# Performance work log

Hardware: AMD Instinct MI355X
Metric: run time of the kernel (lower is better)

The kernel has to match this reference:

```python
import jax, jax.numpy as jnp
import numpy as np

H = 16  # n_heads

def setup_inputs() -> dict:
    key = jax.random.key(0)
    ks = jax.random.split(key, 8)
    B, S, D = 2, 2048, 1024
    q = jax.random.normal(ks[0], (B, S, D), dtype=jnp.float32)
    k = jax.random.normal(ks[1], (B, S, D), dtype=jnp.float32)
    v = jax.random.normal(ks[2], (B, S, D), dtype=jnp.float32)
    mask = jnp.ones((B, S, S), dtype=jnp.int32)
    scale = 1.0 / np.sqrt(D)
    Wq = jax.random.normal(ks[3], (D, D), dtype=jnp.float32) * scale
    Wk = jax.random.normal(ks[4], (D, D), dtype=jnp.float32) * scale
    Wv = jax.random.normal(ks[5], (D, D), dtype=jnp.float32) * scale
    Wo = jax.random.normal(ks[6], (D, D), dtype=jnp.float32) * scale
    return {"q": q, "k": k, "v": v, "mask": mask,
            "Wq": Wq, "Wk": Wk, "Wv": Wv, "Wo": Wo}

def reference(q, k, v, mask, Wq, Wk, Wv, Wo):
    B, S, D = q.shape
    dk = D // H
    # nn.Linear(bias=False): y = x @ W.T
    query = (q @ Wq.T).reshape(B, S, H, dk).transpose(0, 2, 1, 3)  # [B,H,S,dk]
    key_  = (k @ Wk.T).reshape(B, S, H, dk).transpose(0, 2, 1, 3)
    value = (v @ Wv.T).reshape(B, S, H, dk).transpose(0, 2, 1, 3)
    scores = jnp.einsum('bhqd,bhkd->bhqk', query, key_) / jnp.sqrt(jnp.float32(dk))
    scores = jnp.where(mask[:, None, :, :] == 0, jnp.float32(-1e9), scores)
    attn = jax.nn.softmax(scores, axis=-1)  # dropout=0.0 -> identity
    x = jnp.einsum('bhqk,bhkd->bhqd', attn, value)  # [B,H,S,dk]
    x = x.transpose(0, 2, 1, 3).reshape(B, S, D)
    return x @ Wo.T
```

## Files before the change

kernel.cpp:

```cpp
#include <hip/hip_runtime.h>
#include <hip/hip_bf16.h>

#define B_ 2
#define S_ 2048
#define D_ 1024
#define H_ 16

typedef __bf16 bf16x8 __attribute__((ext_vector_type(8)));
typedef __bf16 bf16x4v __attribute__((ext_vector_type(4)));
typedef float f32x4 __attribute__((ext_vector_type(4)));
typedef float f32x16 __attribute__((ext_vector_type(16)));

__device__ __forceinline__ float exp2fast(float x) {
  return __builtin_amdgcn_exp2f(x);
}

__device__ __forceinline__ unsigned short f2bf(float f) {
  unsigned int u = __float_as_uint(f);
  u += 0x7fff + ((u >> 16) & 1);
  return (unsigned short)(u >> 16);
}

__device__ __forceinline__ unsigned int pk2(float x, float y) {
  unsigned int r;
  asm("v_cvt_pk_bf16_f32 %0, %1, %2" : "=v"(r) : "v"(x), "v"(y));
  return r;
}

__device__ __forceinline__ void gload_lds16(const void* g, void* l) {
  __builtin_amdgcn_global_load_lds(
      (const __attribute__((address_space(1))) void*)g,
      (__attribute__((address_space(3))) void*)l, 16, 0, 0);
}

__global__ __launch_bounds__(256) void prep(
    const float* __restrict__ q, const float* __restrict__ k,
    const float* __restrict__ v, const int* __restrict__ mask,
    const float* __restrict__ Wq, const float* __restrict__ Wk,
    const float* __restrict__ Wv, const float* __restrict__ Wo,
    unsigned short* __restrict__ qb, unsigned short* __restrict__ kb,
    unsigned short* __restrict__ vb,
    unsigned short* __restrict__ Wqb, unsigned short* __restrict__ Wkb,
    unsigned short* __restrict__ Wvb, unsigned short* __restrict__ Wob,
    int* __restrict__ flag) {
  const int z = blockIdx.z;
  const int stride = gridDim.x * blockDim.x;
  const int tid0 = blockIdx.x * blockDim.x + threadIdx.x;
  if (z < 3) {
    const float* s = z == 0 ? q : (z == 1 ? k : v);
    unsigned short* d = z == 0 ? qb : (z == 1 ? kb : vb);
    const int n4 = B_ * S_ * D_ / 4;
    for (int i = tid0; i < n4; i += stride) {
      float4 f = ((const float4*)s)[i];
      ushort4 o;
      o.x = f2bf(f.x); o.y = f2bf(f.y); o.z = f2bf(f.z); o.w = f2bf(f.w);
      ((ushort4*)d)[i] = o;
    }
  } else if (z == 3) {
    const int n4 = D_ * D_ / 4;
#pragma unroll
    for (int t = 0; t < 4; t++) {
      const float* s = t == 0 ? Wq : (t == 1 ? Wk : (t == 2 ? Wv : Wo));
      unsigned short* d = t == 0 ? Wqb : (t == 1 ? Wkb : (t == 2 ? Wvb : Wob));
      for (int i = tid0; i < n4; i += stride) {
        float4 f = ((const float4*)s)[i];
        ushort4 o;
        o.x = f2bf(f.x); o.y = f2bf(f.y); o.z = f2bf(f.z); o.w = f2bf(f.w);
        ((ushort4*)d)[i] = o;
      }
    }
  } else {
    const int half = B_ * S_ * S_ / 8;
    const int base = (z - 4) * half;
    bool zf = false;
    for (int i = tid0; i < half; i += stride) {
      int4 mv = ((const int4*)mask)[base + i];
      zf |= (mv.x == 0) || (mv.y == 0) || (mv.z == 0) || (mv.w == 0);
    }
    if (__any(zf)) {
      if ((threadIdx.x & 63) == 0) atomicOr(flag, 1);
    }
  }
}

__device__ __forceinline__ void gemm_core(
    const unsigned short* __restrict__ A, const unsigned short* __restrict__ W,
    unsigned short* As, unsigned short* Bs, int rowBase, int colBase,
    f32x4 (&acc)[4][4]) {
  const int tid = threadIdx.x, lane = tid & 63, w = tid >> 6;
  const int wm = w >> 1, wn = w & 1, l15 = lane & 15, l4 = lane >> 4;
  for (int kt = 0; kt < 16; ++kt) {
#pragma unroll
    for (int i = 0; i < 4; i++) {
      int chunk = (w * 4 + i) * 64 + lane;
      int row = chunk >> 3, c = chunk & 7;
      int cs = c ^ (row & 7);
      gload_lds16(A + (size_t)(rowBase + row) * 1024 + kt * 64 + cs * 8,
                  (char*)As + (w * 4 + i) * 1024);
      gload_lds16(W + (size_t)(colBase + row) * 1024 + kt * 64 + cs * 8,
                  (char*)Bs + (w * 4 + i) * 1024);
    }
    __syncthreads();
#pragma unroll
    for (int ks = 0; ks < 2; ks++) {
      bf16x8 af[4], bfr[4];
#pragma unroll
      for (int mi = 0; mi < 4; mi++) {
        int row = wm * 64 + mi * 16 + l15;
        af[mi] = *(const bf16x8*)((const char*)As + row * 128 +
                                  (((ks * 4 + l4) ^ (row & 7)) << 4));
      }
#pragma unroll
      for (int ni = 0; ni < 4; ni++) {
        int row = wn * 64 + ni * 16 + l15;
        bfr[ni] = *(const bf16x8*)((const char*)Bs + row * 128 +
                                   (((ks * 4 + l4) ^ (row & 7)) << 4));
      }
#pragma unroll
      for (int mi = 0; mi < 4; mi++)
#pragma unroll
        for (int ni = 0; ni < 4; ni++)
          acc[mi][ni] = __builtin_amdgcn_mfma_f32_16x16x32_bf16(
              af[mi], bfr[ni], acc[mi][ni], 0, 0, 0);
    }
    __syncthreads();
  }
}

__global__ __launch_bounds__(256, 2) void gemm_qkv(
    const unsigned short* __restrict__ qA, const unsigned short* __restrict__ kA,
    const unsigned short* __restrict__ vA,
    const unsigned short* __restrict__ Wq, const unsigned short* __restrict__ Wk,
    const unsigned short* __restrict__ Wv,
    unsigned short* __restrict__ Qp, unsigned short* __restrict__ Kp,
    unsigned short* __restrict__ Vtp) {
  __shared__ unsigned short As[128 * 64], Bs[128 * 64];
  const int z = blockIdx.z;
  const unsigned short* A = z == 0 ? qA : (z == 1 ? kA : vA);
  const unsigned short* W = z == 0 ? Wq : (z == 1 ? Wk : Wv);
  const int rowBase = blockIdx.y * 128, colBase = blockIdx.x * 128;
  f32x4 acc[4][4] = {};
  gemm_core(A, W, As, Bs, rowBase, colBase, acc);
  const int tid = threadIdx.x, lane = tid & 63, w = tid >> 6;
  const int wm = w >> 1, wn = w & 1, l15 = lane & 15, l4 = lane >> 4;
#pragma unroll
  for (int mi = 0; mi < 4; mi++)
#pragma unroll
    for (int ni = 0; ni < 4; ni++)
#pragma unroll
      for (int r = 0; r < 4; r++) {
        int gr = rowBase + wm * 64 + mi * 16 + l4 * 4 + r;
        int gc = colBase + wn * 64 + ni * 16 + l15;
        int b = gr >> 11, s = gr & 2047, h = gc >> 6, d = gc & 63;
        float v = acc[mi][ni][r];
        if (z == 0)
          Qp[(((size_t)(b * 16 + h) * 2048 + s) << 6) + d] =
              f2bf(v * 0.18033688011112042f);
        else if (z == 1)
          Kp[(((size_t)(b * 16 + h) * 2048 + s) << 6) + d] = f2bf(v);
        else
          Vtp[((size_t)(b * 16 + h) * 64 + d) * 2048 + s] = f2bf(v);
      }
}

__global__ __launch_bounds__(256, 2) void gemm_o(
    const unsigned short* __restrict__ A, const unsigned short* __restrict__ W,
    float* __restrict__ Out) {
  __shared__ unsigned short As[128 * 64], Bs[128 * 64];
  const int rowBase = blockIdx.y * 128, colBase = blockIdx.x * 128;
  f32x4 acc[4][4] = {};
  gemm_core(A, W, As, Bs, rowBase, colBase, acc);
  const int tid = threadIdx.x, lane = tid & 63, w = tid >> 6;
  const int wm = w >> 1, wn = w & 1, l15 = lane & 15, l4 = lane >> 4;
#pragma unroll
  for (int mi = 0; mi < 4; mi++)
#pragma unroll
    for (int ni = 0; ni < 4; ni++)
#pragma unroll
      for (int r = 0; r < 4; r++) {
        int gr = rowBase + wm * 64 + mi * 16 + l4 * 4 + r;
        int gc = colBase + wn * 64 + ni * 16 + l15;
        Out[(size_t)gr * 1024 + gc] = acc[mi][ni][r];
      }
}

__global__ __launch_bounds__(256, 2) void attn(
    const unsigned short* __restrict__ Qp, const unsigned short* __restrict__ Kp,
    const unsigned short* __restrict__ Vt, unsigned short* __restrict__ Xo,
    const int* __restrict__ flag, const int* __restrict__ mask) {
  __shared__ unsigned short Ks[2][64 * 64];
  __shared__ unsigned short Vs[2][64 * 64];
  const int tid = threadIdx.x, lane = tid & 63, w = tid >> 6;
  const int l31 = lane & 31, hi = lane >> 5;
  const int bid = ((blockIdx.x & 7) << 6) + (blockIdx.x >> 3);
  const int qblk = bid & 15;
  const int bh = bid >> 4;
  const int h = bh & 15, b = bh >> 4;
  const int q = qblk * 128 + w * 32 + l31;
  const int hz = *flag;

  const unsigned short* Kbase = Kp + (size_t)bh * S_ * 64;
  const unsigned short* Vbase = Vt + (size_t)bh * 64 * S_;

  bf16x8 qf[4];
#pragma unroll
  for (int ds = 0; ds < 4; ds++)
    qf[ds] = *(const bf16x8*)(Qp + ((size_t)bh * S_ + q) * 64 + ds * 16 + hi * 8);

  float m = -__builtin_inff(), l = 0.f;
  f32x16 accO[2] = {};

  auto stage = [&](int kt, int buf) {
#pragma unroll
    for (int i = 0; i < 2; i++) {
      int ch = (w * 2 + i) * 64 + lane;
      int row = ch >> 3, c = ch & 7;
      int cs = c ^ (row & 7);
      gload_lds16(Kbase + (size_t)(kt * 64 + row) * 64 + cs * 8,
                  (char*)&Ks[buf][0] + (w * 2 + i) * 1024);
      gload_lds16(Vbase + (size_t)row * S_ + kt * 64 + cs * 8,
                  (char*)&Vs[buf][0] + (w * 2 + i) * 1024);
    }
  };

  stage(0, 0);

  for (int kt = 0; kt < 32; ++kt) {
    const int cur = kt & 1;
    __syncthreads();
    if (kt < 31) stage(kt + 1, cur ^ 1);

    f32x16 s[2] = {};
#pragma unroll
    for (int ds = 0; ds < 4; ds++)
#pragma unroll
      for (int kb = 0; kb < 2; kb++) {
        int row = kb * 32 + l31;
        bf16x8 kf = *(const bf16x8*)((const char*)&Ks[cur][0] + row * 128 +
                                     (((ds * 2 + hi) ^ (row & 7)) << 4));
        s[kb] = __builtin_amdgcn_mfma_f32_32x32x16_bf16(kf, qf[ds], s[kb], 0, 0, 0);
      }

    if (hz) {
#pragma unroll
      for (int kb = 0; kb < 2; kb++)
#pragma unroll
        for (int i = 0; i < 16; i++) {
          int kc = kt * 64 + kb * 32 + (i & 3) + 8 * (i >> 2) + 4 * hi;
          if (mask[((size_t)b * S_ + q) * S_ + kc] == 0) s[kb][i] = -1e9f;
        }
    }

    float mx = s[0][0];
#pragma unroll
    for (int i = 1; i < 16; i++) mx = fmaxf(mx, s[0][i]);
#pragma unroll
    for (int i = 0; i < 16; i++) mx = fmaxf(mx, s[1][i]);
    mx = fmaxf(mx, __shfl_xor(mx, 32));

    if (!__all(mx - m <= 8.f)) {
      float mn = fmaxf(m, mx);
      float al = exp2fast(m - mn);
      m = mn;
      l *= al;
#pragma unroll
      for (int db = 0; db < 2; db++)
#pragma unroll
        for (int i = 0; i < 16; i++) accO[db][i] *= al;
    }

    float rs = 0.f;
#pragma unroll
    for (int kb = 0; kb < 2; kb++)
#pragma unroll
      for (int i = 0; i < 16; i++) {
        float p = exp2fast(s[kb][i] - m);
        s[kb][i] = p;
        rs += p;
      }
    rs += __shfl_xor(rs, 32);
    l += rs;

#pragma unroll
    for (int ks2 = 0; ks2 < 4; ks2++) {
      union { unsigned int u[4]; bf16x8 v; } pb;
      {
        const int kb = ks2 >> 1;
        const int gb = (ks2 & 1) * 8;
        unsigned int a0 = pk2(s[kb][gb + 0], s[kb][gb + 1]);
        unsigned int a1 = pk2(s[kb][gb + 2], s[kb][gb + 3]);
        unsigned int b0 = pk2(s[kb][gb + 4], s[kb][gb + 5]);
        unsigned int b1 = pk2(s[kb][gb + 6], s[kb][gb + 7]);
        unsigned int t0 = hi ? a0 : b0;
        unsigned int t1 = hi ? a1 : b1;
        unsigned int r0 = __shfl_xor(t0, 32);
        unsigned int r1 = __shfl_xor(t1, 32);
        pb.u[0] = hi ? r0 : a0;
        pb.u[1] = hi ? r1 : a1;
        pb.u[2] = hi ? b0 : r0;
        pb.u[3] = hi ? b1 : r1;
      }
#pragma unroll
      for (int db = 0; db < 2; db++) {
        int row = db * 32 + l31;
        bf16x8 vf = *(const bf16x8*)((const char*)&Vs[cur][0] + row * 128 +
                                     (((ks2 * 2 + hi) ^ (row & 7)) << 4));
        accO[db] = __builtin_amdgcn_mfma_f32_32x32x16_bf16(vf, pb.v, accO[db], 0, 0, 0);
      }
    }
  }

  float rl = 1.0f / l;
  const size_t orow = (((size_t)(b * S_ + q)) << 10) + h * 64;
#pragma unroll
  for (int db = 0; db < 2; db++)
#pragma unroll
    for (int rq = 0; rq < 4; rq++) {
      bf16x4v o;
#pragma unroll
      for (int j = 0; j < 4; j++) o[j] = (__bf16)(accO[db][rq * 4 + j] * rl);
      *(bf16x4v*)(Xo + orow + db * 32 + rq * 8 + hi * 4) = o;
    }
}

extern "C" void kernel_launch(void* const* d_in, const int* in_sizes, int n_in,
                              void* d_out, int out_size, void* d_ws, size_t ws_size,
                              hipStream_t stream) {
  const float* q = (const float*)d_in[0];
  const float* k = (const float*)d_in[1];
  const float* v = (const float*)d_in[2];
  const int* mask = (const int*)d_in[3];
  const float* Wq = (const float*)d_in[4];
  const float* Wk = (const float*)d_in[5];
  const float* Wv = (const float*)d_in[6];
  const float* Wo = (const float*)d_in[7];

  char* ws = (char*)d_ws;
  const size_t MB = 1024 * 1024;
  unsigned short* qb16 = (unsigned short*)(ws);
  unsigned short* kb16 = (unsigned short*)(ws + 8 * MB);
  unsigned short* vb16 = (unsigned short*)(ws + 16 * MB);
  unsigned short* Wq16 = (unsigned short*)(ws + 24 * MB);
  unsigned short* Wk16 = (unsigned short*)(ws + 26 * MB);
  unsigned short* Wv16 = (unsigned short*)(ws + 28 * MB);
  unsigned short* Wo16 = (unsigned short*)(ws + 30 * MB);
  unsigned short* Qp = (unsigned short*)(ws + 32 * MB);
  unsigned short* Kp = (unsigned short*)(ws + 40 * MB);
  unsigned short* Vtp = (unsigned short*)(ws + 48 * MB);
  int* flag = (int*)(ws + 56 * MB);
  unsigned short* Xo = qb16;

  (void)hipMemsetAsync(flag, 0, 4, stream);
  prep<<<dim3(1024, 1, 6), 256, 0, stream>>>(q, k, v, mask, Wq, Wk, Wv, Wo,
                                             qb16, kb16, vb16, Wq16, Wk16, Wv16,
                                             Wo16, flag);
  gemm_qkv<<<dim3(8, 32, 3), 256, 0, stream>>>(qb16, kb16, vb16, Wq16, Wk16, Wv16,
                                               Qp, Kp, Vtp);
  attn<<<dim3(512), 256, 0, stream>>>(Qp, Kp, Vtp, Xo, flag, mask);
  gemm_o<<<dim3(8, 32), 256, 0, stream>>>(Xo, Wo16, (float*)d_out);
}
```

Before: 146.5 us.

## Compute softmax row sums via MFMA, unroll attention loop, retile output GEMM

New measurement: 143.7 us. No clear change (-1.9%).

```diff
diff --git a/kernel.cpp b/kernel.cpp
--- a/kernel.cpp
+++ b/kernel.cpp
@@ -13,6 +13,10 @@
 
 __device__ __forceinline__ float exp2fast(float x) {
   return __builtin_amdgcn_exp2f(x);
+}
+
+__device__ __forceinline__ float max3f(float a, float b, float c) {
+  return fmaxf(fmaxf(a, b), c);
 }
 
 __device__ __forceinline__ unsigned short f2bf(float f) {
@@ -166,20 +170,61 @@
 __global__ __launch_bounds__(256, 2) void gemm_o(
     const unsigned short* __restrict__ A, const unsigned short* __restrict__ W,
     float* __restrict__ Out) {
-  __shared__ unsigned short As[128 * 64], Bs[128 * 64];
-  const int rowBase = blockIdx.y * 128, colBase = blockIdx.x * 128;
-  f32x4 acc[4][4] = {};
-  gemm_core(A, W, As, Bs, rowBase, colBase, acc);
+  __shared__ unsigned short As[128 * 64], Bs[64 * 64];
+  const int rowBase = blockIdx.y * 128, colBase = blockIdx.x * 64;
   const int tid = threadIdx.x, lane = tid & 63, w = tid >> 6;
   const int wm = w >> 1, wn = w & 1, l15 = lane & 15, l4 = lane >> 4;
+  f32x4 acc[4][2] = {};
+  for (int kt = 0; kt < 16; ++kt) {
+#pragma unroll
+    for (int i = 0; i < 4; i++) {
+      int chunk = (w * 4 + i) * 64 + lane;
+      int row = chunk >> 3, c = chunk & 7;
+      int cs = c ^ (row & 7);
+      gload_lds16(A + (size_t)(rowBase + row) * 1024 + kt * 64 + cs * 8,
+                  (char*)As + (w * 4 + i) * 1024);
+    }
+#pragma unroll
+    for (int i = 0; i < 2; i++) {
+      int chunk = (w * 2 + i) * 64 + lane;
+      int row = chunk >> 3, c = chunk & 7;
+      int cs = c ^ (row & 7);
+      gload_lds16(W + (size_t)(colBase + row) * 1024 + kt * 64 + cs * 8,
+                  (char*)Bs + (w * 2 + i) * 1024);
+    }
+    __syncthreads();
+#pragma unroll
+    for (int ks = 0; ks < 2; ks++) {
+      bf16x8 af[4], bfr[2];
+#pragma unroll
+      for (int mi = 0; mi < 4; mi++) {
+        int row = wm * 64 + mi * 16 + l15;
+        af[mi] = *(const bf16x8*)((const char*)As + row * 128 +
+                                  (((ks * 4 + l4) ^ (row & 7)) << 4));
+      }
+#pragma unroll
+      for (int ni = 0; ni < 2; ni++) {
+        int row = wn * 32 + ni * 16 + l15;
+        bfr[ni] = *(const bf16x8*)((const char*)Bs + row * 128 +
+                                   (((ks * 4 + l4) ^ (row & 7)) << 4));
+      }
+#pragma unroll
+      for (int mi = 0; mi < 4; mi++)
+#pragma unroll
+        for (int ni = 0; ni < 2; ni++)
+          acc[mi][ni] = __builtin_amdgcn_mfma_f32_16x16x32_bf16(
+              af[mi], bfr[ni], acc[mi][ni], 0, 0, 0);
+    }
+    __syncthreads();
+  }
 #pragma unroll
   for (int mi = 0; mi < 4; mi++)
 #pragma unroll
-    for (int ni = 0; ni < 4; ni++)
+    for (int ni = 0; ni < 2; ni++)
 #pragma unroll
       for (int r = 0; r < 4; r++) {
         int gr = rowBase + wm * 64 + mi * 16 + l4 * 4 + r;
-        int gc = colBase + wn * 64 + ni * 16 + l15;
+        int gc = colBase + wn * 32 + ni * 16 + l15;
         Out[(size_t)gr * 1024 + gc] = acc[mi][ni][r];
       }
 }
@@ -207,7 +252,11 @@
   for (int ds = 0; ds < 4; ds++)
     qf[ds] = *(const bf16x8*)(Qp + ((size_t)bh * S_ + q) * 64 + ds * 16 + hi * 8);
 
-  float m = -__builtin_inff(), l = 0.f;
+  union { unsigned int u[4]; bf16x8 v; } ones;
+  ones.u[0] = ones.u[1] = ones.u[2] = ones.u[3] = 0x3F803F80u;
+
+  float m = -__builtin_inff();
+  f32x16 lsum = {};
   f32x16 accO[2] = {};
 
   auto stage = [&](int kt, int buf) {
@@ -223,23 +272,19 @@
     }
   };
 
-  stage(0, 0);
-
-  for (int kt = 0; kt < 32; ++kt) {
-    const int cur = kt & 1;
-    __syncthreads();
-    if (kt < 31) stage(kt + 1, cur ^ 1);
-
+  auto body = [&](int kt, int cbuf) {
     f32x16 s[2] = {};
+    __builtin_amdgcn_s_setprio(1);
 #pragma unroll
     for (int ds = 0; ds < 4; ds++)
 #pragma unroll
       for (int kb = 0; kb < 2; kb++) {
         int row = kb * 32 + l31;
-        bf16x8 kf = *(const bf16x8*)((const char*)&Ks[cur][0] + row * 128 +
+        bf16x8 kf = *(const bf16x8*)((const char*)&Ks[cbuf][0] + row * 128 +
                                      (((ds * 2 + hi) ^ (row & 7)) << 4));
         s[kb] = __builtin_amdgcn_mfma_f32_32x32x16_bf16(kf, qf[ds], s[kb], 0, 0, 0);
       }
+    __builtin_amdgcn_s_setprio(0);
 
     if (hz) {
 #pragma unroll
@@ -251,35 +296,39 @@
         }
     }
 
-    float mx = s[0][0];
-#pragma unroll
-    for (int i = 1; i < 16; i++) mx = fmaxf(mx, s[0][i]);
-#pragma unroll
-    for (int i = 0; i < 16; i++) mx = fmaxf(mx, s[1][i]);
+    float a0 = max3f(s[0][0], s[0][1], s[0][2]);
+    float a1 = max3f(s[0][3], s[0][4], s[0][5]);
+    float a2 = max3f(s[0][6], s[0][7], s[0][8]);
+    float a3 = max3f(s[0][9], s[0][10], s[0][11]);
+    float a4 = max3f(s[0][12], s[0][13], s[0][14]);
+    float a5 = max3f(s[0][15], s[1][0], s[1][1]);
+    float a6 = max3f(s[1][2], s[1][3], s[1][4]);
+    float a7 = max3f(s[1][5], s[1][6], s[1][7]);
+    float a8 = max3f(s[1][8], s[1][9], s[1][10]);
+    float a9 = max3f(s[1][11], s[1][12], s[1][13]);
+    float aa = fmaxf(s[1][14], s[1][15]);
+    float b0 = max3f(a0, a1, a2);
+    float b1 = max3f(a3, a4, a5);
+    float b2 = max3f(a6, a7, a8);
+    float b3 = max3f(a9, aa, b0);
+    float mx = max3f(b1, b2, b3);
     mx = fmaxf(mx, __shfl_xor(mx, 32));
 
     if (!__all(mx - m <= 8.f)) {
       float mn = fmaxf(m, mx);
       float al = exp2fast(m - mn);
       m = mn;
-      l *= al;
+      lsum[0] *= al;
 #pragma unroll
       for (int db = 0; db < 2; db++)
 #pragma unroll
         for (int i = 0; i < 16; i++) accO[db][i] *= al;
     }
 
-    float rs = 0.f;
 #pragma unroll
     for (int kb = 0; kb < 2; kb++)
 #pragma unroll
-      for (int i = 0; i < 16; i++) {
-        float p = exp2fast(s[kb][i] - m);
-        s[kb][i] = p;
-        rs += p;
-      }
-    rs += __shfl_xor(rs, 32);
-    l += rs;
+      for (int i = 0; i < 16; i++) s[kb][i] = exp2fast(s[kb][i] - m);
 
 #pragma unroll
     for (int ks2 = 0; ks2 < 4; ks2++) {
@@ -287,30 +336,43 @@
       {
         const int kb = ks2 >> 1;
         const int gb = (ks2 & 1) * 8;
-        unsigned int a0 = pk2(s[kb][gb + 0], s[kb][gb + 1]);
-        unsigned int a1 = pk2(s[kb][gb + 2], s[kb][gb + 3]);
-        unsigned int b0 = pk2(s[kb][gb + 4], s[kb][gb + 5]);
-        unsigned int b1 = pk2(s[kb][gb + 6], s[kb][gb + 7]);
-        unsigned int t0 = hi ? a0 : b0;
-        unsigned int t1 = hi ? a1 : b1;
+        unsigned int a0u = pk2(s[kb][gb + 0], s[kb][gb + 1]);
+        unsigned int a1u = pk2(s[kb][gb + 2], s[kb][gb + 3]);
+        unsigned int b0u = pk2(s[kb][gb + 4], s[kb][gb + 5]);
+        unsigned int b1u = pk2(s[kb][gb + 6], s[kb][gb + 7]);
+        unsigned int t0 = hi ? a0u : b0u;
+        unsigned int t1 = hi ? a1u : b1u;
         unsigned int r0 = __shfl_xor(t0, 32);
         unsigned int r1 = __shfl_xor(t1, 32);
-        pb.u[0] = hi ? r0 : a0;
-        pb.u[1] = hi ? r1 : a1;
-        pb.u[2] = hi ? b0 : r0;
-        pb.u[3] = hi ? b1 : r1;
-      }
+        pb.u[0] = hi ? r0 : a0u;
+        pb.u[1] = hi ? r1 : a1u;
+        pb.u[2] = hi ? b0u : r0;
+        pb.u[3] = hi ? b1u : r1;
+      }
+      __builtin_amdgcn_s_setprio(1);
+      lsum = __builtin_amdgcn_mfma_f32_32x32x16_bf16(ones.v, pb.v, lsum, 0, 0, 0);
 #pragma unroll
       for (int db = 0; db < 2; db++) {
         int row = db * 32 + l31;
-        bf16x8 vf = *(const bf16x8*)((const char*)&Vs[cur][0] + row * 128 +
+        bf16x8 vf = *(const bf16x8*)((const char*)&Vs[cbuf][0] + row * 128 +
                                      (((ks2 * 2 + hi) ^ (row & 7)) << 4));
         accO[db] = __builtin_amdgcn_mfma_f32_32x32x16_bf16(vf, pb.v, accO[db], 0, 0, 0);
       }
-    }
+      __builtin_amdgcn_s_setprio(0);
+    }
+  };
+
+  stage(0, 0);
+  for (int kt2 = 0; kt2 < 32; kt2 += 2) {
+    __syncthreads();
+    stage(kt2 + 1, 1);
+    body(kt2, 0);
+    __syncthreads();
+    if (kt2 + 2 < 32) stage(kt2 + 2, 0);
+    body(kt2 + 1, 1);
   }
 
-  float rl = 1.0f / l;
+  float rl = 1.0f / lsum[0];
   const size_t orow = (((size_t)(b * S_ + q)) << 10) + h * 64;
 #pragma unroll
   for (int db = 0; db < 2; db++)
@@ -357,5 +419,5 @@
   gemm_qkv<<<dim3(8, 32, 3), 256, 0, stream>>>(qb16, kb16, vb16, Wq16, Wk16, Wv16,
                                                Qp, Kp, Vtp);
   attn<<<dim3(512), 256, 0, stream>>>(Qp, Kp, Vtp, Xo, flag, mask);
-  gemm_o<<<dim3(8, 32), 256, 0, stream>>>(Xo, Wo16, (float*)d_out);
-}
+  gemm_o<<<dim3(16, 32), 256, 0, stream>>>(Xo, Wo16, (float*)d_out);
+}
```
